# Kernel optimization log

Hardware: AMD Instinct MI355X
Metric: run time of the kernel (lower is better)

Reference implementation:

```python
import jax, jax.numpy as jnp
import numpy as np

IN_F, OUT_F, RANK = 4096, 4096, 16
ALPHA = 32.0
SCALING = ALPHA / RANK


def setup_inputs() -> dict:
    key = jax.random.key(0)
    kx, kw, ka, kb = jax.random.split(key, 4)
    x = jax.random.normal(kx, (4, 2048, IN_F), dtype=jnp.float32)
    # base linear weight [out, in] (kaiming-uniform-like scale)
    bound_w = 1.0 / np.sqrt(IN_F)
    W = jax.random.uniform(kw, (OUT_F, IN_F), minval=-bound_w, maxval=bound_w, dtype=jnp.float32)
    # lora_A [rank, in]: kaiming uniform; lora_B [out, rank]: nonzero for testing
    bound_a = np.sqrt(6.0 / IN_F) / np.sqrt(1.0 + 5.0)
    lora_A = jax.random.uniform(ka, (RANK, IN_F), minval=-bound_a, maxval=bound_a, dtype=jnp.float32)
    lora_B = jax.random.normal(kb, (OUT_F, RANK), dtype=jnp.float32) * 0.02
    return {"x": x, "W": W, "lora_A": lora_A, "lora_B": lora_B}


def reference(x, W, lora_A, lora_B):
    # base: x @ W^T  -> [b, s, out]
    base = jnp.einsum("bsi,oi->bso", x, W)
    # low-rank path: (x @ A^T) @ B^T * scaling (dropout p=0 -> identity)
    r = jnp.einsum("bsi,ri->bsr", x, lora_A)  # [b, s, rank]
    lora = jnp.einsum("bsr,or->bso", r, lora_B) * SCALING
    return base + lora
```

## Files before the change

### kernel.cpp

```cpp
#include <hip/hip_runtime.h>
#include <stdint.h>
#include <stddef.h>

#define IN_F    4096
#define OUT_F   4096
#define MTOK    8192
#define RANK    16
#define SCALING 2.0f

typedef __attribute__((ext_vector_type(8))) short          bf16x8;
typedef __attribute__((ext_vector_type(4))) float          f32x4;
typedef __attribute__((ext_vector_type(4))) float          fl4;
typedef __attribute__((ext_vector_type(4))) unsigned short u16x4;
typedef __attribute__((ext_vector_type(8))) unsigned short u16x8;

static __device__ __forceinline__ unsigned short f2bf(float f) {
  union { float f; uint32_t u; } v; v.f = f;
  return (unsigned short)((v.u + 0x7fffu + ((v.u >> 16) & 1u)) >> 16);
}

static __device__ __forceinline__ void gload16(const void* g, void* l) {
  __builtin_amdgcn_global_load_lds(
      (const __attribute__((address_space(1))) uint32_t*)g,
      (__attribute__((address_space(3))) uint32_t*)l,
      16, 0, 0);
}

__global__ void merge_w_kernel(const float* __restrict__ W,
                               const float* __restrict__ lA,
                               const float* __restrict__ lB,
                               unsigned short* __restrict__ Weff) {
  __shared__ float Bs[RANK];
  const int o = blockIdx.x;
  if (threadIdx.x < RANK) Bs[threadIdx.x] = lB[o * RANK + threadIdx.x] * SCALING;
  __syncthreads();
  for (int c = threadIdx.x * 4; c < IN_F; c += 256 * 4) {
    fl4 w = *(const fl4*)(W + (size_t)o * IN_F + c);
#pragma unroll
    for (int r = 0; r < RANK; ++r) {
      const float b = Bs[r];
      const fl4 a = *(const fl4*)(lA + (size_t)r * IN_F + c);
      w[0] += b * a[0]; w[1] += b * a[1]; w[2] += b * a[2]; w[3] += b * a[3];
    }
    u16x4 p;
    p[0] = f2bf(w[0]); p[1] = f2bf(w[1]); p[2] = f2bf(w[2]); p[3] = f2bf(w[3]);
    *(u16x4*)(Weff + (size_t)o * IN_F + c) = p;
  }
}

__global__ void conv_x_kernel(const float* __restrict__ x,
                              unsigned short* __restrict__ xb) {
  const size_t i = ((size_t)blockIdx.x * 256 + threadIdx.x) * 8;
  const fl4 a = *(const fl4*)(x + i);
  const fl4 b = *(const fl4*)(x + i + 4);
  u16x8 p;
  p[0] = f2bf(a[0]); p[1] = f2bf(a[1]); p[2] = f2bf(a[2]); p[3] = f2bf(a[3]);
  p[4] = f2bf(b[0]); p[5] = f2bf(b[1]); p[6] = f2bf(b[2]); p[7] = f2bf(b[3]);
  *(u16x8*)(xb + i) = p;
}

__global__ __launch_bounds__(512, 2) void gemm8p_kernel(
    const unsigned short* __restrict__ X,
    const unsigned short* __restrict__ Wf,
    float* __restrict__ Out) {
  __shared__ char lds[131072];
  const int tid  = threadIdx.x;
  const int lane = tid & 63;
  const int wave = tid >> 6;
  const int wr = wave >> 2;
  const int wc = wave & 3;
  const int fr = lane & 15;
  const int fq = lane >> 4;

  const int bid = blockIdx.x;
  const int swz = (bid & 7) * 64 + (bid >> 3);
  const int tm = swz & 31;
  const int tn = swz >> 5;
  const int m0 = tm << 8;
  const int n0 = tn << 8;

  const unsigned short* Ag = X  + (size_t)m0 * IN_F;
  const unsigned short* Bg = Wf + (size_t)n0 * IN_F;

  const int rIW = lane >> 3;
  const int csw = ((lane & 7) ^ rIW) << 3;

  const int aBase = wr * 16384 + fr * 128;
  const int bBase = 65536 + (wc >> 1) * 16384 + (wc & 1) * 8192 + fr * 128;
  const int cA0 = (fq << 4) ^ ((fr & 7) << 4);
  const int cA1 = cA0 ^ 64;

#define STAGE_A(C, BUF, K) do {                                                \
    const int _rh = (C) * 64 + (wave & 3) * 16;                                \
    const int _r0 = (wave >> 2) * 128 + _rh + rIW;                             \
    char* _d = lds + (BUF) * 32768 + (wave >> 2) * 16384 + _rh * 128 +         \
               (lane << 4);                                                    \
    gload16(Ag + (size_t)_r0 * IN_F + (K) + csw, _d);                          \
    gload16(Ag + (size_t)(_r0 + 8) * IN_F + (K) + csw, _d + 1024);             \
  } while (0)

#define STAGE_B(C, BUF, K) do {                                                \
    const int _s  = wave >> 1;                                                 \
    const int _rh = (_s & 1) * 64 + (C) * 32 + (wave & 1) * 16;                \
    const int _r0 = (_s >> 1) * 128 + _rh + rIW;                               \
    char* _d = lds + 65536 + (BUF) * 32768 + (_s >> 1) * 16384 + _rh * 128 +   \
               (lane << 4);                                                    \
    gload16(Bg + (size_t)_r0 * IN_F + (K) + csw, _d);                          \
    gload16(Bg + (size_t)(_r0 + 8) * IN_F + (K) + csw, _d + 1024);             \
  } while (0)

#define LDA(BUF, M, KK) (*(const bf16x8*)(lds + (BUF) * 32768 + aBase + (M) * 2048 + (KK)))
#define LDB(BUF, N, KK) (*(const bf16x8*)(lds + (BUF) * 32768 + bBase + (N) * 2048 + (KK)))

  f32x4 acc[8][4];
#pragma unroll
  for (int i = 0; i < 8; ++i)
#pragma unroll
    for (int j = 0; j < 4; ++j) acc[i][j] = (f32x4){0.f, 0.f, 0.f, 0.f};

  bf16x8 a[8], b0[4], b1[4];

  STAGE_B(0, 0, 0); STAGE_B(1, 0, 0); STAGE_A(0, 0, 0); STAGE_A(1, 0, 0);

  for (int t = 0; t < 64; ++t) {
    const int bu = t & 1;
    const int nb = bu ^ 1;
    const int kn = (t + 1) << 6;
    const bool pf = (t + 1 < 64);

    if (pf) {
      STAGE_B(0, nb, kn);
      asm volatile("s_waitcnt vmcnt(4)" ::: "memory");
    } else {
      asm volatile("s_waitcnt vmcnt(2)" ::: "memory");
    }
    __builtin_amdgcn_s_barrier();
#pragma unroll
    for (int mi = 0; mi < 4; ++mi) { a[mi*2] = LDA(bu, mi, cA0); a[mi*2+1] = LDA(bu, mi, cA1); }
#pragma unroll
    for (int ni = 0; ni < 2; ++ni) { b0[ni*2] = LDB(bu, ni, cA0); b0[ni*2+1] = LDB(bu, ni, cA1); }
    __builtin_amdgcn_s_setprio(1);
#pragma unroll
    for (int mi = 0; mi < 4; ++mi)
#pragma unroll
      for (int ni = 0; ni < 2; ++ni) {
        acc[mi][ni] = __builtin_amdgcn_mfma_f32_16x16x32_bf16(a[mi*2],   b0[ni*2],   acc[mi][ni], 0, 0, 0);
        acc[mi][ni] = __builtin_amdgcn_mfma_f32_16x16x32_bf16(a[mi*2+1], b0[ni*2+1], acc[mi][ni], 0, 0, 0);
      }
    __builtin_amdgcn_s_setprio(0);
#pragma unroll
    for (int ni = 0; ni < 2; ++ni) { b1[ni*2] = LDB(bu, 2+ni, cA0); b1[ni*2+1] = LDB(bu, 2+ni, cA1); }
    __builtin_amdgcn_s_barrier();

    if (pf) {
      STAGE_B(1, nb, kn);
      asm volatile("s_waitcnt vmcnt(4)" ::: "memory");
    } else {
      asm volatile("s_waitcnt vmcnt(0)" ::: "memory");
    }
    __builtin_amdgcn_s_barrier();
    __builtin_amdgcn_s_setprio(1);
#pragma unroll
    for (int mi = 0; mi < 4; ++mi)
#pragma unroll
      for (int ni = 0; ni < 2; ++ni) {
        acc[mi][2+ni] = __builtin_amdgcn_mfma_f32_16x16x32_bf16(a[mi*2],   b1[ni*2],   acc[mi][2+ni], 0, 0, 0);
        acc[mi][2+ni] = __builtin_amdgcn_mfma_f32_16x16x32_bf16(a[mi*2+1], b1[ni*2+1], acc[mi][2+ni], 0, 0, 0);
      }
    __builtin_amdgcn_s_setprio(0);
#pragma unroll
    for (int mi = 0; mi < 4; ++mi) { a[mi*2] = LDA(bu, 4+mi, cA0); a[mi*2+1] = LDA(bu, 4+mi, cA1); }
    __builtin_amdgcn_s_barrier();

    if (pf) STAGE_A(0, nb, kn);
    __builtin_amdgcn_s_barrier();
    __builtin_amdgcn_s_setprio(1);
#pragma unroll
    for (int mi = 0; mi < 4; ++mi)
#pragma unroll
      for (int ni = 0; ni < 2; ++ni) {
        acc[4+mi][2+ni] = __builtin_amdgcn_mfma_f32_16x16x32_bf16(a[mi*2],   b1[ni*2],   acc[4+mi][2+ni], 0, 0, 0);
        acc[4+mi][2+ni] = __builtin_amdgcn_mfma_f32_16x16x32_bf16(a[mi*2+1], b1[ni*2+1], acc[4+mi][2+ni], 0, 0, 0);
      }
    __builtin_amdgcn_s_setprio(0);
#pragma unroll
    for (int ni = 0; ni < 2; ++ni) { b0[ni*2] = LDB(bu, ni, cA0); b0[ni*2+1] = LDB(bu, ni, cA1); }
    __builtin_amdgcn_s_barrier();

    if (pf) STAGE_A(1, nb, kn);
    __builtin_amdgcn_s_barrier();
    __builtin_amdgcn_s_setprio(1);
#pragma unroll
    for (int mi = 0; mi < 4; ++mi)
#pragma unroll
      for (int ni = 0; ni < 2; ++ni) {
        acc[4+mi][ni] = __builtin_amdgcn_mfma_f32_16x16x32_bf16(a[mi*2],   b0[ni*2],   acc[4+mi][ni], 0, 0, 0);
        acc[4+mi][ni] = __builtin_amdgcn_mfma_f32_16x16x32_bf16(a[mi*2+1], b0[ni*2+1], acc[4+mi][ni], 0, 0, 0);
      }
    __builtin_amdgcn_s_setprio(0);
    __builtin_amdgcn_s_barrier();
  }

#pragma unroll
  for (int mi = 0; mi < 8; ++mi) {
    const int row0 = m0 + wr * 128 + mi * 16 + fq * 4;
#pragma unroll
    for (int ni = 0; ni < 4; ++ni) {
      const int col = n0 + wc * 64 + ni * 16 + fr;
#pragma unroll
      for (int j = 0; j < 4; ++j)
        Out[(size_t)(row0 + j) * OUT_F + col] = acc[mi][ni][j];
    }
  }
#undef STAGE_A
#undef STAGE_B
#undef LDA
#undef LDB
}

__global__ __launch_bounds__(256) void gemm_f32x_kernel(
    const float* __restrict__ X,
    const unsigned short* __restrict__ Weff,
    float* __restrict__ Out) {
  __shared__ unsigned short As[128][32];
  __shared__ unsigned short Bs[128][32];

  const int tid  = threadIdx.x;
  const int lane = tid & 63;
  const int wave = tid >> 6;
  const int wr = wave >> 1, wc = wave & 1;
  const int fr = lane & 15, fq = lane >> 4;

  const int bid = blockIdx.x;
  const int m0 = (bid & 63) * 128;
  const int n0 = (bid >> 6) * 128;

  f32x4 acc[4][4];
#pragma unroll
  for (int i = 0; i < 4; ++i)
#pragma unroll
    for (int j = 0; j < 4; ++j) acc[i][j] = (f32x4){0.f, 0.f, 0.f, 0.f};

  const int srow = tid >> 2;
  const int sseg = tid & 3;

  for (int k0 = 0; k0 < IN_F; k0 += 32) {
    if (k0) __syncthreads();
    {
      const unsigned short* gB = Weff + (size_t)(n0 + srow) * IN_F + k0 + sseg * 8;
      gload16(gB, &Bs[srow][sseg * 8]);
      gload16(gB + (size_t)64 * IN_F, &Bs[64 + srow][sseg * 8]);
    }
#pragma unroll
    for (int it = 0; it < 4; ++it) {
      const int c   = tid + it * 256;
      const int row = c >> 3;
      const int c4  = (c & 7) * 4;
      const fl4 v = *(const fl4*)(X + (size_t)(m0 + row) * IN_F + k0 + c4);
      u16x4 p;
      p[0] = f2bf(v[0]); p[1] = f2bf(v[1]); p[2] = f2bf(v[2]); p[3] = f2bf(v[3]);
      *(u16x4*)&As[row][c4] = p;
    }
    __syncthreads();

    bf16x8 af[4], bfm[4];
#pragma unroll
    for (int m = 0; m < 4; ++m)
      af[m] = *(const bf16x8*)&As[wr * 64 + m * 16 + fr][fq * 8];
#pragma unroll
    for (int n = 0; n < 4; ++n)
      bfm[n] = *(const bf16x8*)&Bs[wc * 64 + n * 16 + fr][fq * 8];
#pragma unroll
    for (int m = 0; m < 4; ++m)
#pragma unroll
      for (int n = 0; n < 4; ++n)
        acc[m][n] = __builtin_amdgcn_mfma_f32_16x16x32_bf16(af[m], bfm[n], acc[m][n], 0, 0, 0);
  }

#pragma unroll
  for (int m = 0; m < 4; ++m) {
    const int row0 = m0 + wr * 64 + m * 16 + fq * 4;
#pragma unroll
    for (int n = 0; n < 4; ++n) {
      const int col = n0 + wc * 64 + n * 16 + fr;
#pragma unroll
      for (int j = 0; j < 4; ++j)
        Out[(size_t)(row0 + j) * OUT_F + col] = acc[m][n][j];
    }
  }
}

__global__ void lora_r_kernel(const float* __restrict__ x,
                              const float* __restrict__ lA,
                              float* __restrict__ r) {
  const int idx = blockIdx.x * 256 + threadIdx.x;
  const int m = idx / RANK, rr = idx % RANK;
  float acc = 0.f;
  for (int k = 0; k < IN_F; ++k)
    acc += x[(size_t)m * IN_F + k] * lA[(size_t)rr * IN_F + k];
  r[idx] = acc * SCALING;
}

__global__ void naive_out_kernel(const float* __restrict__ x,
                                 const float* __restrict__ W,
                                 const float* __restrict__ lB,
                                 const float* __restrict__ r,
                                 float* __restrict__ out) {
  const size_t idx = (size_t)blockIdx.x * 256 + threadIdx.x;
  const int m = (int)(idx / OUT_F), n = (int)(idx % OUT_F);
  float acc = 0.f;
  for (int k = 0; k < IN_F; ++k)
    acc += x[(size_t)m * IN_F + k] * W[(size_t)n * IN_F + k];
#pragma unroll
  for (int rr = 0; rr < RANK; ++rr)
    acc += r[(size_t)m * RANK + rr] * lB[(size_t)n * RANK + rr];
  out[idx] = acc;
}

extern "C" void kernel_launch(void* const* d_in, const int* in_sizes, int n_in,
                              void* d_out, int out_size, void* d_ws, size_t ws_size,
                              hipStream_t stream) {
  const float* x  = (const float*)d_in[0];
  const float* W  = (const float*)d_in[1];
  const float* lA = (const float*)d_in[2];
  const float* lB = (const float*)d_in[3];
  float* out = (float*)d_out;

  const size_t weff_bytes = (size_t)OUT_F * IN_F * 2;
  const size_t xb_bytes   = (size_t)MTOK * IN_F * 2;

  if (ws_size >= weff_bytes + xb_bytes) {
    unsigned short* Weff = (unsigned short*)d_ws;
    unsigned short* xb   = (unsigned short*)((char*)d_ws + weff_bytes);
    merge_w_kernel<<<OUT_F, 256, 0, stream>>>(W, lA, lB, Weff);
    conv_x_kernel<<<(MTOK * (size_t)IN_F) / (256 * 8), 256, 0, stream>>>(x, xb);
    gemm8p_kernel<<<(MTOK / 256) * (OUT_F / 256), 512, 0, stream>>>(xb, Weff, out);
  } else if (ws_size >= weff_bytes) {
    unsigned short* Weff = (unsigned short*)d_ws;
    merge_w_kernel<<<OUT_F, 256, 0, stream>>>(W, lA, lB, Weff);
    gemm_f32x_kernel<<<(MTOK / 128) * (OUT_F / 128), 256, 0, stream>>>(x, Weff, out);
  } else {
    float* r = (float*)d_ws;
    lora_r_kernel<<<(MTOK * RANK) / 256, 256, 0, stream>>>(x, lA, r);
    naive_out_kernel<<<(size_t)MTOK * OUT_F / 256, 256, 0, stream>>>(x, W, lB, r, out);
  }
}
```

Baseline: 340.9 us.

## Fuse weight merge and x conversion, remap tile order, unroll k-loop by two

Merges the weight-merge and x-to-bf16 conversion kernels into a single prep kernel that dispatches on block index, removing one launch and letting both jobs run concurrently. Changes the GEMM block-to-tile mapping so groups of consecutive blocks cover a 4x8 patch of M tiles sharing N columns, which is meant to improve L2 reuse. Manually unrolls the k-loop by two with constant buffer indices so LDS offsets become compile-time constants. Risks include register pressure from the larger unrolled body and a different cache-locality pattern.

```diff
diff --git a/kernel.cpp b/kernel.cpp
--- a/kernel.cpp
+++ b/kernel.cpp
@@ -26,37 +26,38 @@
       16, 0, 0);
 }
 
-__global__ void merge_w_kernel(const float* __restrict__ W,
-                               const float* __restrict__ lA,
-                               const float* __restrict__ lB,
-                               unsigned short* __restrict__ Weff) {
+__global__ void prep_kernel(const float* __restrict__ x,
+                            const float* __restrict__ W,
+                            const float* __restrict__ lA,
+                            const float* __restrict__ lB,
+                            unsigned short* __restrict__ Weff,
+                            unsigned short* __restrict__ xb) {
   __shared__ float Bs[RANK];
-  const int o = blockIdx.x;
-  if (threadIdx.x < RANK) Bs[threadIdx.x] = lB[o * RANK + threadIdx.x] * SCALING;
-  __syncthreads();
-  for (int c = threadIdx.x * 4; c < IN_F; c += 256 * 4) {
-    fl4 w = *(const fl4*)(W + (size_t)o * IN_F + c);
-#pragma unroll
-    for (int r = 0; r < RANK; ++r) {
-      const float b = Bs[r];
-      const fl4 a = *(const fl4*)(lA + (size_t)r * IN_F + c);
-      w[0] += b * a[0]; w[1] += b * a[1]; w[2] += b * a[2]; w[3] += b * a[3];
-    }
-    u16x4 p;
-    p[0] = f2bf(w[0]); p[1] = f2bf(w[1]); p[2] = f2bf(w[2]); p[3] = f2bf(w[3]);
-    *(u16x4*)(Weff + (size_t)o * IN_F + c) = p;
-  }
-}
-
-__global__ void conv_x_kernel(const float* __restrict__ x,
-                              unsigned short* __restrict__ xb) {
-  const size_t i = ((size_t)blockIdx.x * 256 + threadIdx.x) * 8;
-  const fl4 a = *(const fl4*)(x + i);
-  const fl4 b = *(const fl4*)(x + i + 4);
-  u16x8 p;
-  p[0] = f2bf(a[0]); p[1] = f2bf(a[1]); p[2] = f2bf(a[2]); p[3] = f2bf(a[3]);
-  p[4] = f2bf(b[0]); p[5] = f2bf(b[1]); p[6] = f2bf(b[2]); p[7] = f2bf(b[3]);
-  *(u16x8*)(xb + i) = p;
+  if (blockIdx.x < OUT_F) {
+    const int o = blockIdx.x;
+    if (threadIdx.x < RANK) Bs[threadIdx.x] = lB[o * RANK + threadIdx.x] * SCALING;
+    __syncthreads();
+    for (int c = threadIdx.x * 4; c < IN_F; c += 256 * 4) {
+      fl4 w = *(const fl4*)(W + (size_t)o * IN_F + c);
+#pragma unroll
+      for (int r = 0; r < RANK; ++r) {
+        const float b = Bs[r];
+        const fl4 a = *(const fl4*)(lA + (size_t)r * IN_F + c);
+        w[0] += b * a[0]; w[1] += b * a[1]; w[2] += b * a[2]; w[3] += b * a[3];
+      }
+      u16x4 p;
+      p[0] = f2bf(w[0]); p[1] = f2bf(w[1]); p[2] = f2bf(w[2]); p[3] = f2bf(w[3]);
+      *(u16x4*)(Weff + (size_t)o * IN_F + c) = p;
+    }
+  } else {
+    const size_t i = ((size_t)(blockIdx.x - OUT_F) * 256 + threadIdx.x) * 8;
+    const fl4 a = *(const fl4*)(x + i);
+    const fl4 b = *(const fl4*)(x + i + 4);
+    u16x8 p;
+    p[0] = f2bf(a[0]); p[1] = f2bf(a[1]); p[2] = f2bf(a[2]); p[3] = f2bf(a[3]);
+    p[4] = f2bf(b[0]); p[5] = f2bf(b[1]); p[6] = f2bf(b[2]); p[7] = f2bf(b[3]);
+    *(u16x8*)(xb + i) = p;
+  }
 }
 
 __global__ __launch_bounds__(512, 2) void gemm8p_kernel(
@@ -73,9 +74,8 @@
   const int fq = lane >> 4;
 
   const int bid = blockIdx.x;
-  const int swz = (bid & 7) * 64 + (bid >> 3);
-  const int tm = swz & 31;
-  const int tn = swz >> 5;
+  const int tm  = (bid & 7) * 4 + ((bid >> 3) & 3);
+  const int tn  = bid >> 5;
   const int m0 = tm << 8;
   const int n0 = tn << 8;
 
@@ -112,6 +112,59 @@
 #define LDA(BUF, M, KK) (*(const bf16x8*)(lds + (BUF) * 32768 + aBase + (M) * 2048 + (KK)))
 #define LDB(BUF, N, KK) (*(const bf16x8*)(lds + (BUF) * 32768 + bBase + (N) * 2048 + (KK)))
 
+#define MFMA_Q(MB, NB, BR)                                                     \
+  _Pragma("unroll")                                                            \
+  for (int mi = 0; mi < 4; ++mi)                                               \
+    _Pragma("unroll")                                                          \
+    for (int ni = 0; ni < 2; ++ni) {                                           \
+      acc[(MB)+mi][(NB)+ni] = __builtin_amdgcn_mfma_f32_16x16x32_bf16(a[mi*2],   BR[ni*2],   acc[(MB)+mi][(NB)+ni], 0, 0, 0); \
+      acc[(MB)+mi][(NB)+ni] = __builtin_amdgcn_mfma_f32_16x16x32_bf16(a[mi*2+1], BR[ni*2+1], acc[(MB)+mi][(NB)+ni], 0, 0, 0); \
+    }
+
+#define TILE(BU, NB, KN, PF)                                                   \
+  do {                                                                         \
+                                                    \
+    if (PF) { STAGE_B(0, NB, KN);                                              \
+              asm volatile("s_waitcnt vmcnt(4)" ::: "memory"); }               \
+    else    { asm volatile("s_waitcnt vmcnt(2)" ::: "memory"); }               \
+    __builtin_amdgcn_s_barrier();                                              \
+    _Pragma("unroll")                                                          \
+    for (int mi = 0; mi < 4; ++mi) { a[mi*2] = LDA(BU, mi, cA0); a[mi*2+1] = LDA(BU, mi, cA1); } \
+    _Pragma("unroll")                                                          \
+    for (int ni = 0; ni < 2; ++ni) { b0[ni*2] = LDB(BU, ni, cA0); b0[ni*2+1] = LDB(BU, ni, cA1); } \
+    __builtin_amdgcn_s_setprio(1);                                             \
+    MFMA_Q(0, 0, b0)                                                           \
+    __builtin_amdgcn_s_setprio(0);                                             \
+    _Pragma("unroll")                                                          \
+    for (int ni = 0; ni < 2; ++ni) { b1[ni*2] = LDB(BU, 2+ni, cA0); b1[ni*2+1] = LDB(BU, 2+ni, cA1); } \
+    __builtin_amdgcn_s_barrier();                                              \
+                                                    \
+    if (PF) { STAGE_B(1, NB, KN);                                              \
+              asm volatile("s_waitcnt vmcnt(4)" ::: "memory"); }               \
+    else    { asm volatile("s_waitcnt vmcnt(0)" ::: "memory"); }               \
+    __builtin_amdgcn_s_barrier();                                              \
+    __builtin_amdgcn_s_setprio(1);                                             \
+    MFMA_Q(0, 2, b1)                                                           \
+    __builtin_amdgcn_s_setprio(0);                                             \
+    _Pragma("unroll")                                                          \
+    for (int mi = 0; mi < 4; ++mi) { a[mi*2] = LDA(BU, 4+mi, cA0); a[mi*2+1] = LDA(BU, 4+mi, cA1); } \
+    __builtin_amdgcn_s_barrier();                                              \
+                                                    \
+    if (PF) STAGE_A(0, NB, KN);                                                \
+    __builtin_amdgcn_s_barrier();                                              \
+    __builtin_amdgcn_s_setprio(1);                                             \
+    MFMA_Q(4, 2, b1)                                                           \
+    __builtin_amdgcn_s_setprio(0);                                             \
+    __builtin_amdgcn_s_barrier();                                              \
+                                                    \
+    if (PF) STAGE_A(1, NB, KN);                                                \
+    __builtin_amdgcn_s_barrier();                                              \
+    __builtin_amdgcn_s_setprio(1);                                             \
+    MFMA_Q(4, 0, b0)                                                           \
+    __builtin_amdgcn_s_setprio(0);                                             \
+    __builtin_amdgcn_s_barrier();                                              \
+  } while (0)
+
   f32x4 acc[8][4];
 #pragma unroll
   for (int i = 0; i < 8; ++i)
@@ -122,83 +175,11 @@
 
   STAGE_B(0, 0, 0); STAGE_B(1, 0, 0); STAGE_A(0, 0, 0); STAGE_A(1, 0, 0);
 
-  for (int t = 0; t < 64; ++t) {
-    const int bu = t & 1;
-    const int nb = bu ^ 1;
-    const int kn = (t + 1) << 6;
-    const bool pf = (t + 1 < 64);
-
-    if (pf) {
-      STAGE_B(0, nb, kn);
-      asm volatile("s_waitcnt vmcnt(4)" ::: "memory");
-    } else {
-      asm volatile("s_waitcnt vmcnt(2)" ::: "memory");
-    }
-    __builtin_amdgcn_s_barrier();
-#pragma unroll
-    for (int mi = 0; mi < 4; ++mi) { a[mi*2] = LDA(bu, mi, cA0); a[mi*2+1] = LDA(bu, mi, cA1); }
-#pragma unroll
-    for (int ni = 0; ni < 2; ++ni) { b0[ni*2] = LDB(bu, ni, cA0); b0[ni*2+1] = LDB(bu, ni, cA1); }
-    __builtin_amdgcn_s_setprio(1);
-#pragma unroll
-    for (int mi = 0; mi < 4; ++mi)
-#pragma unroll
-      for (int ni = 0; ni < 2; ++ni) {
-        acc[mi][ni] = __builtin_amdgcn_mfma_f32_16x16x32_bf16(a[mi*2],   b0[ni*2],   acc[mi][ni], 0, 0, 0);
-        acc[mi][ni] = __builtin_amdgcn_mfma_f32_16x16x32_bf16(a[mi*2+1], b0[ni*2+1], acc[mi][ni], 0, 0, 0);
-      }
-    __builtin_amdgcn_s_setprio(0);
-#pragma unroll
-    for (int ni = 0; ni < 2; ++ni) { b1[ni*2] = LDB(bu, 2+ni, cA0); b1[ni*2+1] = LDB(bu, 2+ni, cA1); }
-    __builtin_amdgcn_s_barrier();
-
-    if (pf) {
-      STAGE_B(1, nb, kn);
-      asm volatile("s_waitcnt vmcnt(4)" ::: "memory");
-    } else {
-      asm volatile("s_waitcnt vmcnt(0)" ::: "memory");
-    }
-    __builtin_amdgcn_s_barrier();
-    __builtin_amdgcn_s_setprio(1);
-#pragma unroll
-    for (int mi = 0; mi < 4; ++mi)
-#pragma unroll
-      for (int ni = 0; ni < 2; ++ni) {
-        acc[mi][2+ni] = __builtin_amdgcn_mfma_f32_16x16x32_bf16(a[mi*2],   b1[ni*2],   acc[mi][2+ni], 0, 0, 0);
-        acc[mi][2+ni] = __builtin_amdgcn_mfma_f32_16x16x32_bf16(a[mi*2+1], b1[ni*2+1], acc[mi][2+ni], 0, 0, 0);
-      }
-    __builtin_amdgcn_s_setprio(0);
-#pragma unroll
-    for (int mi = 0; mi < 4; ++mi) { a[mi*2] = LDA(bu, 4+mi, cA0); a[mi*2+1] = LDA(bu, 4+mi, cA1); }
-    __builtin_amdgcn_s_barrier();
-
-    if (pf) STAGE_A(0, nb, kn);
-    __builtin_amdgcn_s_barrier();
-    __builtin_amdgcn_s_setprio(1);
-#pragma unroll
-    for (int mi = 0; mi < 4; ++mi)
-#pragma unroll
-      for (int ni = 0; ni < 2; ++ni) {
-        acc[4+mi][2+ni] = __builtin_amdgcn_mfma_f32_16x16x32_bf16(a[mi*2],   b1[ni*2],   acc[4+mi][2+ni], 0, 0, 0);
-        acc[4+mi][2+ni] = __builtin_amdgcn_mfma_f32_16x16x32_bf16(a[mi*2+1], b1[ni*2+1], acc[4+mi][2+ni], 0, 0, 0);
-      }
-    __builtin_amdgcn_s_setprio(0);
-#pragma unroll
-    for (int ni = 0; ni < 2; ++ni) { b0[ni*2] = LDB(bu, ni, cA0); b0[ni*2+1] = LDB(bu, ni, cA1); }
-    __builtin_amdgcn_s_barrier();
-
-    if (pf) STAGE_A(1, nb, kn);
-    __builtin_amdgcn_s_barrier();
-    __builtin_amdgcn_s_setprio(1);
-#pragma unroll
-    for (int mi = 0; mi < 4; ++mi)
-#pragma unroll
-      for (int ni = 0; ni < 2; ++ni) {
-        acc[4+mi][ni] = __builtin_amdgcn_mfma_f32_16x16x32_bf16(a[mi*2],   b0[ni*2],   acc[4+mi][ni], 0, 0, 0);
-        acc[4+mi][ni] = __builtin_amdgcn_mfma_f32_16x16x32_bf16(a[mi*2+1], b0[ni*2+1], acc[4+mi][ni], 0, 0, 0);
-      }
-    __builtin_amdgcn_s_setprio(0);
-    __builtin_amdgcn_s_barrier();
+  for (int tt = 0; tt < 32; ++tt) {
+    const int k1 = (tt << 7) + 64;
+    const int k2 = k1 + 64;
+    TILE(0, 1, k1, true);
+    TILE(1, 0, k2, (k2 < IN_F));
   }
 
 #pragma unroll
@@ -216,6 +197,8 @@
 #undef STAGE_B
 #undef LDA
 #undef LDB
+#undef MFMA_Q
+#undef TILE
 }
 
 __global__ __launch_bounds__(256) void gemm_f32x_kernel(
@@ -332,12 +315,12 @@
   if (ws_size >= weff_bytes + xb_bytes) {
     unsigned short* Weff = (unsigned short*)d_ws;
     unsigned short* xb   = (unsigned short*)((char*)d_ws + weff_bytes);
-    merge_w_kernel<<<OUT_F, 256, 0, stream>>>(W, lA, lB, Weff);
-    conv_x_kernel<<<(MTOK * (size_t)IN_F) / (256 * 8), 256, 0, stream>>>(x, xb);
+    const int conv_blocks = (int)((MTOK * (size_t)IN_F) / (256 * 8));
+    prep_kernel<<<OUT_F + conv_blocks, 256, 0, stream>>>(x, W, lA, lB, Weff, xb);
     gemm8p_kernel<<<(MTOK / 256) * (OUT_F / 256), 512, 0, stream>>>(xb, Weff, out);
   } else if (ws_size >= weff_bytes) {
     unsigned short* Weff = (unsigned short*)d_ws;
-    merge_w_kernel<<<OUT_F, 256, 0, stream>>>(W, lA, lB, Weff);
+    prep_kernel<<<OUT_F, 256, 0, stream>>>(x, W, lA, lB, Weff, (unsigned short*)0);
     gemm_f32x_kernel<<<(MTOK / 128) * (OUT_F / 128), 256, 0, stream>>>(x, Weff, out);
   } else {
     float* r = (float*)d_ws;
```

Measured after the change: 303.6 us. 1.12x faster.
